# Performance work log

Hardware: AMD Instinct MI355X
Metric: run time of the kernel (lower is better)

Reference implementation:

```python
import jax, jax.numpy as jnp
import numpy as np

S, B, C = 7, 2, 20
E = B * 5 + C  # 30
BATCH = 16384


def setup_inputs() -> dict:
    key = jax.random.key(0)
    k1, k2, k3 = jax.random.split(key, 3)
    # keep coords in [0.05, 0.95) so sqrt(w,h) stays well-defined (original would NaN on negatives)
    pred = 0.05 + 0.9 * jax.random.uniform(k1, (BATCH, S, S, E), dtype=jnp.float32)
    tgt = 0.05 + 0.9 * jax.random.uniform(k2, (BATCH, S, S, E), dtype=jnp.float32)
    conf = (jax.random.uniform(k3, (BATCH, S, S)) < 0.3).astype(jnp.float32)
    # both per-cell boxes carry the same objectness target (channels 4 and 9), exactly 0 or 1
    tgt = tgt.at[..., 4].set(conf).at[..., 9].set(conf)
    return {"pred_tensor": pred, "target_tensor": tgt}


def _iou_vs_first(pb, t0):
    # pb: [..., B, 4], t0: [..., 4]; boxes treated as raw corners [x1,y1,x2,y2]
    # (faithful to original compute_iou which does NOT convert xywh -> corners)
    t = t0[..., None, :]  # [..., 1, 4]
    lt = jnp.maximum(pb[..., :2], t[..., :2])
    rb = jnp.minimum(pb[..., 2:4], t[..., 2:4])
    wh = jnp.maximum(rb - lt, 0.0)
    inter = wh[..., 0] * wh[..., 1]                            # [..., B]
    a1 = (pb[..., 2] - pb[..., 0]) * (pb[..., 3] - pb[..., 1])  # [..., B]
    a2 = (t[..., 2] - t[..., 0]) * (t[..., 3] - t[..., 1])      # [..., 1]
    return inter / (a1 + a2 - inter)


def reference(pred_tensor, target_tensor):
    dt = pred_tensor.dtype
    m = (target_tensor[..., 4] > 0).astype(dt)    # obj cell mask  [N,S,S]
    nm = (target_tensor[..., 4] == 0).astype(dt)  # noobj cell mask [N,S,S]

    lead = pred_tensor.shape[:3]
    pb = pred_tensor[..., : B * 5].reshape(*lead, B, 5)    # [N,S,S,B,5]
    tb = target_tensor[..., : B * 5].reshape(*lead, B, 5)  # [N,S,S,B,5]

    # IoU of each predicted box vs the FIRST target box of the cell (box_target[i] in the loop)
    iou = _iou_vs_first(pb[..., :4], tb[..., 0, :4])  # [N,S,S,B]
    max_iou = jnp.max(iou, axis=-1)                   # [N,S,S]
    resp = jax.nn.one_hot(jnp.argmax(iou, axis=-1), B, dtype=dt)  # responsible-box mask [N,S,S,B]
    w = m[..., None] * resp                           # per-box responsibility weight

    loss_xy = jnp.sum(w * jnp.sum((pb[..., :2] - tb[..., :2]) ** 2, axis=-1))
    loss_wh = jnp.sum(w * jnp.sum((jnp.sqrt(pb[..., 2:4]) - jnp.sqrt(tb[..., 2:4])) ** 2, axis=-1))
    # original stores max_iou via .data -> detached target
    loss_obj = jnp.sum(w * (pb[..., 4] - jax.lax.stop_gradient(max_iou)[..., None]) ** 2)
    loss_noobj = jnp.sum(nm * ((pred_tensor[..., 4] - target_tensor[..., 4]) ** 2
                               + (pred_tensor[..., 9] - target_tensor[..., 9]) ** 2))
    loss_class = jnp.sum(m[..., None] * (pred_tensor[..., B * 5:] - target_tensor[..., B * 5:]) ** 2)
    return (loss_xy, loss_wh, loss_obj, loss_noobj, loss_class)
```

## Files before the change

kernel.cpp:

```cpp
#include <hip/hip_runtime.h>

constexpr int S = 7, NB = 2, C = 20, E = 30;
constexpr int BATCH = 16384;
constexpr int NCELLS = BATCH * S * S;

__global__ void zero_out_kernel(float* out) {
    if (threadIdx.x < 5) out[threadIdx.x] = 0.0f;
}

__global__ __launch_bounds__(256, 4) void yolo_loss_kernel(
    const float* __restrict__ pred,
    const float* __restrict__ tgt,
    float* __restrict__ out)
{
    const int tid      = blockIdx.x * blockDim.x + threadIdx.x;
    const int nthreads = gridDim.x * blockDim.x;
    const int lane     = threadIdx.x & 63;
    const int wv       = threadIdx.x >> 6;

    float acc0 = 0.f, acc1 = 0.f, acc2 = 0.f, acc3 = 0.f, acc4 = 0.f;

    for (int cell = tid; cell < NCELLS; cell += nthreads) {
        const float2* gp = reinterpret_cast<const float2*>(pred) + (size_t)cell * 15;
        const float2* gt = reinterpret_cast<const float2*>(tgt)  + (size_t)cell * 15;

        float p[30], t[30];
        #pragma unroll
        for (int j = 0; j < 15; ++j) {
            float2 a = gp[j]; p[2*j] = a.x; p[2*j+1] = a.y;
        }
        #pragma unroll
        for (int j = 0; j < 15; ++j) {
            float2 b = gt[j]; t[2*j] = b.x; t[2*j+1] = b.y;
        }

        const float tconf = t[4];
        const float m  = (tconf > 0.0f)  ? 1.0f : 0.0f;
        const float nm = 1.0f - m;

        const float t0x1 = t[0], t0y1 = t[1], t0x2 = t[2], t0y2 = t[3];
        const float a2 = (t0x2 - t0x1) * (t0y2 - t0y1);

        float iou[2];
        #pragma unroll
        for (int b = 0; b < 2; ++b) {
            const float px1 = p[5*b+0], py1 = p[5*b+1];
            const float px2 = p[5*b+2], py2 = p[5*b+3];
            const float ltx = fmaxf(px1, t0x1), lty = fmaxf(py1, t0y1);
            const float rbx = fminf(px2, t0x2), rby = fminf(py2, t0y2);
            const float wx = fmaxf(rbx - ltx, 0.0f), wy = fmaxf(rby - lty, 0.0f);
            const float inter = wx * wy;
            const float a1 = (px2 - px1) * (py2 - py1);
            iou[b] = inter / (a1 + a2 - inter);
        }

        const float max_iou = fmaxf(iou[0], iou[1]);
        const int r = (iou[0] >= iou[1]) ? 0 : 5;

        {
            const float dx = p[r+0] - t[r+0];
            const float dy = p[r+1] - t[r+1];
            acc0 += m * (dx*dx + dy*dy);
        }
        {
            const float dw = sqrtf(p[r+2]) - sqrtf(t[r+2]);
            const float dh = sqrtf(p[r+3]) - sqrtf(t[r+3]);
            acc1 += m * (dw*dw + dh*dh);
        }
        {
            const float d = p[r+4] - max_iou;
            acc2 += m * d * d;
        }
        {
            const float d0 = p[4] - t[4];
            const float d1 = p[9] - t[9];
            acc3 += nm * (d0*d0 + d1*d1);
        }
        {
            float cl = 0.f;
            #pragma unroll
            for (int k = 10; k < 30; ++k) {
                const float d = p[k] - t[k];
                cl += d * d;
            }
            acc4 += m * cl;
        }
    }

    float acc[5] = {acc0, acc1, acc2, acc3, acc4};
    __shared__ float wave_sums[4][5];
    #pragma unroll
    for (int i = 0; i < 5; ++i) {
        float v = acc[i];
        #pragma unroll
        for (int o = 32; o > 0; o >>= 1)
            v += __shfl_down(v, o, 64);
        if (lane == 0) wave_sums[wv][i] = v;
    }
    __syncthreads();

    if (threadIdx.x < 5) {
        const float v = wave_sums[0][threadIdx.x] + wave_sums[1][threadIdx.x]
                      + wave_sums[2][threadIdx.x] + wave_sums[3][threadIdx.x];
        atomicAdd(out + threadIdx.x, v);
    }
}

extern "C" void kernel_launch(void* const* d_in, const int* in_sizes, int n_in,
                              void* d_out, int out_size, void* d_ws, size_t ws_size,
                              hipStream_t stream) {
    const float* pred = (const float*)d_in[0];
    const float* tgt  = (const float*)d_in[1];
    float* out = (float*)d_out;

    hipLaunchKernelGGL(zero_out_kernel, dim3(1), dim3(64), 0, stream, out);

    hipLaunchKernelGGL(yolo_loss_kernel, dim3(1024), dim3(256), 0, stream,
                       pred, tgt, out);
}
```

Baseline: 218.1 us.

## Process cell pairs per thread with float4 loads and one-shot grid

```diff
diff --git a/kernel.cpp b/kernel.cpp
--- a/kernel.cpp
+++ b/kernel.cpp
@@ -3,88 +3,116 @@
 constexpr int S = 7, NB = 2, C = 20, E = 30;
 constexpr int BATCH = 16384;
 constexpr int NCELLS = BATCH * S * S;
+constexpr int NPAIRS = NCELLS / 2;
 
 __global__ void zero_out_kernel(float* out) {
     if (threadIdx.x < 5) out[threadIdx.x] = 0.0f;
 }
 
-__global__ __launch_bounds__(256, 4) void yolo_loss_kernel(
+__global__ __launch_bounds__(256) void yolo_loss_kernel(
     const float* __restrict__ pred,
     const float* __restrict__ tgt,
     float* __restrict__ out)
 {
-    const int tid      = blockIdx.x * blockDim.x + threadIdx.x;
-    const int nthreads = gridDim.x * blockDim.x;
-    const int lane     = threadIdx.x & 63;
-    const int wv       = threadIdx.x >> 6;
+    const int pair = blockIdx.x * blockDim.x + threadIdx.x;
+    const int lane = threadIdx.x & 63;
+    const int wv   = threadIdx.x >> 6;
 
     float acc0 = 0.f, acc1 = 0.f, acc2 = 0.f, acc3 = 0.f, acc4 = 0.f;
 
-    for (int cell = tid; cell < NCELLS; cell += nthreads) {
-        const float2* gp = reinterpret_cast<const float2*>(pred) + (size_t)cell * 15;
-        const float2* gt = reinterpret_cast<const float2*>(tgt)  + (size_t)cell * 15;
+    if (pair < NPAIRS) {
+        const float4* gp = reinterpret_cast<const float4*>(pred + (size_t)pair * 60);
+        const float4* gt = reinterpret_cast<const float4*>(tgt  + (size_t)pair * 60);
 
-        float p[30], t[30];
+        float p[60], t[60];
         #pragma unroll
         for (int j = 0; j < 15; ++j) {
-            float2 a = gp[j]; p[2*j] = a.x; p[2*j+1] = a.y;
+            float4 a = gp[j];
+            p[4*j+0] = a.x; p[4*j+1] = a.y; p[4*j+2] = a.z; p[4*j+3] = a.w;
         }
         #pragma unroll
         for (int j = 0; j < 15; ++j) {
-            float2 b = gt[j]; t[2*j] = b.x; t[2*j+1] = b.y;
+            float4 b = gt[j];
+            t[4*j+0] = b.x; t[4*j+1] = b.y; t[4*j+2] = b.z; t[4*j+3] = b.w;
         }
 
-        const float tconf = t[4];
-        const float m  = (tconf > 0.0f)  ? 1.0f : 0.0f;
-        const float nm = 1.0f - m;
-
-        const float t0x1 = t[0], t0y1 = t[1], t0x2 = t[2], t0y2 = t[3];
-        const float a2 = (t0x2 - t0x1) * (t0y2 - t0y1);
-
-        float iou[2];
-        #pragma unroll
-        for (int b = 0; b < 2; ++b) {
-            const float px1 = p[5*b+0], py1 = p[5*b+1];
-            const float px2 = p[5*b+2], py2 = p[5*b+3];
-            const float ltx = fmaxf(px1, t0x1), lty = fmaxf(py1, t0y1);
-            const float rbx = fminf(px2, t0x2), rby = fminf(py2, t0y2);
-            const float wx = fmaxf(rbx - ltx, 0.0f), wy = fmaxf(rby - lty, 0.0f);
-            const float inter = wx * wy;
-            const float a1 = (px2 - px1) * (py2 - py1);
-            iou[b] = inter / (a1 + a2 - inter);
+        #define CELL_LOSS(OFF)                                                     \
+        {                                                                          \
+            const float tconf = t[(OFF)+4];                \
+            const float m  = (tconf > 0.0f) ? 1.0f : 0.0f;                         \
+            const float nm = 1.0f - m;                                             \
+            const float t0x1 = t[(OFF)+0], t0y1 = t[(OFF)+1];                      \
+            const float t0x2 = t[(OFF)+2], t0y2 = t[(OFF)+3];                      \
+            const float a2 = (t0x2 - t0x1) * (t0y2 - t0y1);                        \
+            float iou0, iou1;                                                      \
+            {                                                                      \
+                const float ltx = fmaxf(p[(OFF)+0], t0x1);                         \
+                const float lty = fmaxf(p[(OFF)+1], t0y1);                         \
+                const float rbx = fminf(p[(OFF)+2], t0x2);                         \
+                const float rby = fminf(p[(OFF)+3], t0y2);                         \
+                const float wx = fmaxf(rbx - ltx, 0.0f);                           \
+                const float wy = fmaxf(rby - lty, 0.0f);                           \
+                const float inter = wx * wy;                                       \
+                const float a1 = (p[(OFF)+2] - p[(OFF)+0])                         \
+                               * (p[(OFF)+3] - p[(OFF)+1]);                        \
+                iou0 = inter / (a1 + a2 - inter);                                  \
+            }                                                                      \
+            {                                                                      \
+                const float ltx = fmaxf(p[(OFF)+5], t0x1);                         \
+                const float lty = fmaxf(p[(OFF)+6], t0y1);                         \
+                const float rbx = fminf(p[(OFF)+7], t0x2);                         \
+                const float rby = fminf(p[(OFF)+8], t0y2);                         \
+                const float wx = fmaxf(rbx - ltx, 0.0f);                           \
+                const float wy = fmaxf(rby - lty, 0.0f);                           \
+                const float inter = wx * wy;                                       \
+                const float a1 = (p[(OFF)+7] - p[(OFF)+5])                         \
+                               * (p[(OFF)+8] - p[(OFF)+6]);                        \
+                iou1 = inter / (a1 + a2 - inter);                                  \
+            }                                                                      \
+            const float max_iou = fmaxf(iou0, iou1);                               \
+            const bool b1 = iou1 > iou0;                \
+            const float rpx = b1 ? p[(OFF)+5] : p[(OFF)+0];                        \
+            const float rpy = b1 ? p[(OFF)+6] : p[(OFF)+1];                        \
+            const float rpw = b1 ? p[(OFF)+7] : p[(OFF)+2];                        \
+            const float rph = b1 ? p[(OFF)+8] : p[(OFF)+3];                        \
+            const float rpc = b1 ? p[(OFF)+9] : p[(OFF)+4];                        \
+            const float rtx = b1 ? t[(OFF)+5] : t[(OFF)+0];                        \
+            const float rty = b1 ? t[(OFF)+6] : t[(OFF)+1];                        \
+            const float rtw = b1 ? t[(OFF)+7] : t[(OFF)+2];                        \
+            const float rth = b1 ? t[(OFF)+8] : t[(OFF)+3];                        \
+            {                                                              \
+                const float dx = rpx - rtx;                                        \
+                const float dy = rpy - rty;                                        \
+                acc0 += m * (dx*dx + dy*dy);                                       \
+            }                                                                      \
+            {                      \
+                const float dw = sqrtf(rpw) - sqrtf(rtw);                          \
+                const float dh = sqrtf(rph) - sqrtf(rth);                          \
+                acc1 += m * (dw*dw + dh*dh);                                       \
+            }                                                                      \
+            {                                                             \
+                const float d = rpc - max_iou;                                     \
+                acc2 += m * d * d;                                                 \
+            }                                                                      \
+            {                                            \
+                const float d0 = p[(OFF)+4] - t[(OFF)+4];                          \
+                const float d1 = p[(OFF)+9] - t[(OFF)+9];                          \
+                acc3 += nm * (d0*d0 + d1*d1);                                      \
+            }                                                                      \
+            {                                          \
+                float cl = 0.f;                                                    \
+                _Pragma("unroll")                                                  \
+                for (int k = 10; k < 30; ++k) {                                    \
+                    const float d = p[(OFF)+k] - t[(OFF)+k];                       \
+                    cl += d * d;                                                   \
+                }                                                                  \
+                acc4 += m * cl;                                                    \
+            }                                                                      \
         }
 
-        const float max_iou = fmaxf(iou[0], iou[1]);
-        const int r = (iou[0] >= iou[1]) ? 0 : 5;
-
-        {
-            const float dx = p[r+0] - t[r+0];
-            const float dy = p[r+1] - t[r+1];
-            acc0 += m * (dx*dx + dy*dy);
-        }
-        {
-            const float dw = sqrtf(p[r+2]) - sqrtf(t[r+2]);
-            const float dh = sqrtf(p[r+3]) - sqrtf(t[r+3]);
-            acc1 += m * (dw*dw + dh*dh);
-        }
-        {
-            const float d = p[r+4] - max_iou;
-            acc2 += m * d * d;
-        }
-        {
-            const float d0 = p[4] - t[4];
-            const float d1 = p[9] - t[9];
-            acc3 += nm * (d0*d0 + d1*d1);
-        }
-        {
-            float cl = 0.f;
-            #pragma unroll
-            for (int k = 10; k < 30; ++k) {
-                const float d = p[k] - t[k];
-                cl += d * d;
-            }
-            acc4 += m * cl;
-        }
+        CELL_LOSS(0)
+        CELL_LOSS(30)
+        #undef CELL_LOSS
     }
 
     float acc[5] = {acc0, acc1, acc2, acc3, acc4};
@@ -115,6 +143,6 @@
 
     hipLaunchKernelGGL(zero_out_kernel, dim3(1), dim3(64), 0, stream, out);
 
-    hipLaunchKernelGGL(yolo_loss_kernel, dim3(1024), dim3(256), 0, stream,
+    hipLaunchKernelGGL(yolo_loss_kernel, dim3(1568), dim3(256), 0, stream,
                        pred, tgt, out);
 }
```

After: 213.9 us. No clear change (-1.9%).
